# Kernel optimization log

Hardware: AMD Instinct MI355X
Metric: run time of the kernel (lower is better)

## Reference

```python
import jax, jax.numpy as jnp
import numpy as np

B, L, D, H, W = 2, 1024, 1024, 16, 64  # batch, length, dim, num_head, band_width
DH = D // H  # head_dim = 64


def setup_inputs() -> dict:
    key = jax.random.key(0)
    ks = jax.random.split(key, 7)
    scale = 0.02
    return {
        "x": jax.random.normal(ks[0], (B, L, D), dtype=jnp.float32),
        "Wq": jax.random.normal(ks[1], (D, D), dtype=jnp.float32) * scale,
        "Wk": jax.random.normal(ks[2], (D, D), dtype=jnp.float32) * scale,
        "Wv": jax.random.normal(ks[3], (D, D), dtype=jnp.float32) * scale,
        "Wo": jax.random.normal(ks[4], (D, D), dtype=jnp.float32) * scale,
        "last_k_init": jax.random.normal(ks[5], (W - 1, H, DH), dtype=jnp.float32),
        "last_v_init": jax.random.normal(ks[6], (W - 1, H, DH), dtype=jnp.float32),
    }


def reference(x, Wq, Wk, Wv, Wo, last_k_init, last_v_init):
    b, l, d = x.shape
    w1, h, dh = last_k_init.shape  # band_width-1, num_head, head_dim
    w = w1 + 1

    # torch nn.Linear: y = x @ W.T (no bias)
    q = (x @ Wq.T).reshape(b, l, h, dh)
    k = (x @ Wk.T).reshape(b, l, h, dh)
    v = (x @ Wv.T).reshape(b, l, h, dh)

    # prepend learned initial cache (fresh state: last_k is None)
    last_k = jnp.broadcast_to(last_k_init[None], (b, w1, h, dh))
    last_v = jnp.broadcast_to(last_v_init[None], (b, w1, h, dh))
    k_pad = jnp.concatenate([last_k, k], axis=1)  # [b, l+w-1, h, dh]
    v_pad = jnp.concatenate([last_v, v], axis=1)

    # query at position t attends offsets i in [0, w): key index t + i in padded
    # array == original position t - (w-1) + i  (causal sliding window of width w)
    idx = jnp.arange(l)[:, None] + jnp.arange(w)[None, :]  # [l, w]
    k_win = k_pad[:, idx]  # [b, l, w, h, dh]
    v_win = v_pad[:, idx]  # [b, l, w, h, dh]

    scores = jnp.einsum('blhd,blwhd->blwh', q, k_win) * (dh ** -0.5)
    attn = jax.nn.softmax(scores, axis=2)  # softmax over band offsets
    out = jnp.einsum('blwh,blwhd->blhd', attn, v_win).reshape(b, l, d)
    return out @ Wo.T
```

## Files before the change

### kernel.cpp

```cpp
#include <hip/hip_runtime.h>
#include <hip/hip_bf16.h>
#include <stdint.h>

#define B_ 2
#define L_ 1024
#define D_ 1024
#define H_ 16
#define W_ 64
#define DH_ 64

typedef __attribute__((ext_vector_type(8))) __bf16 bf16x8;
typedef __attribute__((ext_vector_type(4))) float floatx4;

#define AS3(p) ((__attribute__((address_space(3))) void*)(p))
#define AS1(p) ((const __attribute__((address_space(1))) void*)(p))

static __device__ __forceinline__ ushort f2bf(float f) {
    union { float f; uint32_t u; } v{f};
    uint32_t r = v.u + 0x7fff + ((v.u >> 16) & 1);
    return (ushort)(r >> 16);
}
static __device__ __forceinline__ uint32_t pack2(float a, float b) {
    return (uint32_t)f2bf(a) | ((uint32_t)f2bf(b) << 16);
}

__global__ __launch_bounds__(256) void cvt_inputs(
    const float* __restrict__ x, const float* __restrict__ wq, const float* __restrict__ wk,
    const float* __restrict__ wv, const float* __restrict__ wo,
    ushort* __restrict__ xb, ushort* __restrict__ wqb, ushort* __restrict__ wkb,
    ushort* __restrict__ wvb, ushort* __restrict__ wob) {
    const size_t M1 = 1u << 20;
    size_t i4 = ((size_t)blockIdx.x * 256 + threadIdx.x) * 4;
    const float* s; ushort* d; size_t off;
    if (i4 < 2 * M1)      { s = x;  d = xb;  off = i4; }
    else if (i4 < 3 * M1) { s = wq; d = wqb; off = i4 - 2 * M1; }
    else if (i4 < 4 * M1) { s = wk; d = wkb; off = i4 - 3 * M1; }
    else if (i4 < 5 * M1) { s = wv; d = wvb; off = i4 - 4 * M1; }
    else                  { s = wo; d = wob; off = i4 - 5 * M1; }
    float4 f = *(const float4*)(s + off);
    ushort4 o;
    o.x = f2bf(f.x); o.y = f2bf(f.y); o.z = f2bf(f.z); o.w = f2bf(f.w);
    *(ushort4*)(d + off) = o;
}

#define BK 64

__global__ __launch_bounds__(256) void gemm_qkv(
    const ushort* __restrict__ xb,
    const ushort* __restrict__ wqb, const ushort* __restrict__ wkb, const ushort* __restrict__ wvb,
    ushort* __restrict__ q, ushort* __restrict__ k, ushort* __restrict__ v) {
    __shared__ __align__(16) ushort As[128 * BK];
    __shared__ __align__(16) ushort Bs[64 * BK];
    const int tid = threadIdx.x;
    const int m0 = blockIdx.x * 128;
    const int nt = blockIdx.y;
    const int which = nt >> 4;
    const int n0 = (nt & 15) * 64;
    const ushort* wsel = which == 0 ? wqb : (which == 1 ? wkb : wvb);
    ushort* dsel = which == 0 ? q : (which == 1 ? k : v);

    const int lane = tid & 63;
    const int wv_ = tid >> 6;
    const int wm = (wv_ & 1) * 64;
    const int wn = (wv_ >> 1) * 32;
    const int lr = lane & 15;
    const int quad = lane >> 4;

    floatx4 acc[4][2];
#pragma unroll
    for (int i = 0; i < 4; ++i)
#pragma unroll
        for (int j = 0; j < 2; ++j) acc[i][j] = (floatx4){0.f, 0.f, 0.f, 0.f};

    int offA[4], offB[2];
#pragma unroll
    for (int it = 0; it < 4; ++it) {
        int c = tid + it * 256;
        int r = c >> 3, s = c & 7, g = s ^ (r & 7);
        offA[it] = (m0 + r) * 1024 + g * 8;
    }
#pragma unroll
    for (int it = 0; it < 2; ++it) {
        int c = tid + it * 256;
        int r = c >> 3, s = c & 7, g = s ^ (r & 7);
        offB[it] = (n0 + r) * 1024 + g * 8;
    }

    for (int k0 = 0; k0 < 1024; k0 += BK) {
#pragma unroll
        for (int it = 0; it < 4; ++it)
            __builtin_amdgcn_global_load_lds(AS1(xb + offA[it] + k0), AS3(As + (it * 256 + tid) * 8), 16, 0, 0);
#pragma unroll
        for (int it = 0; it < 2; ++it)
            __builtin_amdgcn_global_load_lds(AS1(wsel + offB[it] + k0), AS3(Bs + (it * 256 + tid) * 8), 16, 0, 0);
        __syncthreads();
#pragma unroll
        for (int ks = 0; ks < 2; ++ks) {
            bf16x8 af[4], bfr[2];
#pragma unroll
            for (int i = 0; i < 4; ++i) {
                int r = wm + i * 16 + lr;
                af[i] = *(const bf16x8*)(As + r * BK + (((ks * 4 + quad) ^ (r & 7)) * 8));
            }
#pragma unroll
            for (int j = 0; j < 2; ++j) {
                int r = wn + j * 16 + lr;
                bfr[j] = *(const bf16x8*)(Bs + r * BK + (((ks * 4 + quad) ^ (r & 7)) * 8));
            }
#pragma unroll
            for (int i = 0; i < 4; ++i)
#pragma unroll
                for (int j = 0; j < 2; ++j)
                    acc[i][j] = __builtin_amdgcn_mfma_f32_16x16x32_bf16(af[i], bfr[j], acc[i][j], 0, 0, 0);
        }
        __syncthreads();
    }

#pragma unroll
    for (int i = 0; i < 4; ++i) {
        int rbase = m0 + wm + i * 16 + quad * 4;
#pragma unroll
        for (int j = 0; j < 2; ++j) {
            int c = n0 + wn + j * 16 + lr;
            int h = c >> 6, dh = c & 63;
#pragma unroll
            for (int r = 0; r < 4; ++r) {
                int m = rbase + r;
                int bb = m >> 10, l = m & 1023;
                dsel[(((size_t)bb * 16 + h) * 1024 + l) * 64 + dh] = f2bf(acc[i][j][r]);
            }
        }
    }
}

__global__ __launch_bounds__(256) void gemm_wo(
    const ushort* __restrict__ ab,
    const ushort* __restrict__ wob,
    float* __restrict__ out) {
    __shared__ __align__(16) ushort As[64 * BK];
    __shared__ __align__(16) ushort Bs[64 * BK];
    const int tid = threadIdx.x;
    const int m0 = blockIdx.x * 64;
    const int n0 = blockIdx.y * 64;
    const int lane = tid & 63;
    const int wv_ = tid >> 6;
    const int wm = wv_ * 16;
    const int lr = lane & 15;
    const int quad = lane >> 4;

    floatx4 acc[4];
#pragma unroll
    for (int j = 0; j < 4; ++j) acc[j] = (floatx4){0.f, 0.f, 0.f, 0.f};

    int offA[2], offB[2];
#pragma unroll
    for (int it = 0; it < 2; ++it) {
        int c = tid + it * 256;
        int r = c >> 3, s = c & 7, g = s ^ (r & 7);
        offA[it] = (m0 + r) * 1024 + g * 8;
        offB[it] = (n0 + r) * 1024 + g * 8;
    }

    for (int k0 = 0; k0 < 1024; k0 += BK) {
#pragma unroll
        for (int it = 0; it < 2; ++it)
            __builtin_amdgcn_global_load_lds(AS1(ab + offA[it] + k0), AS3(As + (it * 256 + tid) * 8), 16, 0, 0);
#pragma unroll
        for (int it = 0; it < 2; ++it)
            __builtin_amdgcn_global_load_lds(AS1(wob + offB[it] + k0), AS3(Bs + (it * 256 + tid) * 8), 16, 0, 0);
        __syncthreads();
#pragma unroll
        for (int ks = 0; ks < 2; ++ks) {
            int ra = wm + lr;
            bf16x8 af = *(const bf16x8*)(As + ra * BK + (((ks * 4 + quad) ^ (ra & 7)) * 8));
            bf16x8 bfr[4];
#pragma unroll
            for (int j = 0; j < 4; ++j) {
                int r = j * 16 + lr;
                bfr[j] = *(const bf16x8*)(Bs + r * BK + (((ks * 4 + quad) ^ (r & 7)) * 8));
            }
#pragma unroll
            for (int j = 0; j < 4; ++j)
                acc[j] = __builtin_amdgcn_mfma_f32_16x16x32_bf16(af, bfr[j], acc[j], 0, 0, 0);
        }
        __syncthreads();
    }

#pragma unroll
    for (int j = 0; j < 4; ++j) {
        int c = n0 + j * 16 + lr;
#pragma unroll
        for (int r = 0; r < 4; ++r) {
            int m = m0 + wm + quad * 4 + r;
            out[(size_t)m * 1024 + c] = acc[j][r];
        }
    }
}

#define STRQ 72
#define STRV 136

__global__ __launch_bounds__(256) void band_attn3(
    const ushort* __restrict__ q,
    const ushort* __restrict__ k,
    const ushort* __restrict__ v,
    const float* __restrict__ lastk,
    const float* __restrict__ lastv,
    ushort* __restrict__ ao) {
    __shared__ __align__(16) ushort Qs[64 * STRQ];
    __shared__ __align__(16) ushort Kw[128 * STRQ];
    __shared__ __align__(16) ushort Vt[64 * STRV];
    __shared__ __align__(16) ushort Ps[64 * STRV];
    const int tid = threadIdx.x;
    const int lane = tid & 63;
    const int wid = tid >> 6;
    const int l0 = blockIdx.x * 64;
    const int b = blockIdx.y >> 4, h = blockIdx.y & 15;
    const size_t hb = (size_t)(b * 16 + h) * 1024 * 64;

#pragma unroll
    for (int it = 0; it < 2; ++it) {
        int c = tid + it * 256;
        int rr = c >> 3, cc = (c & 7) * 8;
        *(uint4*)(Qs + rr * STRQ + cc) = *(const uint4*)(q + hb + (size_t)(l0 + rr) * 64 + cc);
    }
#pragma unroll
    for (int it = 0; it < 4; ++it) {
        int c = tid + it * 256;
        int j = c >> 3, cc = (c & 7) * 8;
        int pos = l0 + j - 63;
        uint4 t = {0u, 0u, 0u, 0u};
        if (j < 127) {
            if (pos >= 0) {
                t = *(const uint4*)(k + hb + (size_t)pos * 64 + cc);
            } else {
                const float* sk = lastk + ((size_t)j * 16 + h) * 64 + cc;
                float4 a0 = *(const float4*)sk, a1 = *(const float4*)(sk + 4);
                t.x = pack2(a0.x, a0.y); t.y = pack2(a0.z, a0.w);
                t.z = pack2(a1.x, a1.y); t.w = pack2(a1.z, a1.w);
            }
        }
        *(uint4*)(Kw + j * STRQ + cc) = t;
    }
#pragma unroll
    for (int it = 0; it < 4; ++it) {
        int c = tid + it * 256;
        int j = c >> 3, d8 = (c & 7) * 8;
        int pos = l0 + j - 63;
        ushort tv[8];
        if (j >= 127) {
#pragma unroll
            for (int t = 0; t < 8; ++t) tv[t] = 0;
        } else if (pos >= 0) {
            union { uint4 u4; ushort us[8]; } tu;
            tu.u4 = *(const uint4*)(v + hb + (size_t)pos * 64 + d8);
#pragma unroll
            for (int t = 0; t < 8; ++t) tv[t] = tu.us[t];
        } else {
            const float* sv = lastv + ((size_t)j * 16 + h) * 64 + d8;
#pragma unroll
            for (int t = 0; t < 8; ++t) tv[t] = f2bf(sv[t]);
        }
#pragma unroll
        for (int t = 0; t < 8; ++t) Vt[(size_t)(d8 + t) * STRV + j] = tv[t];
    }
    __syncthreads();

    const int lr = lane & 15;
    const int quad = lane >> 4;

    floatx4 sa[8];
#pragma unroll
    for (int nt = 0; nt < 8; ++nt) sa[nt] = (floatx4){0.f, 0.f, 0.f, 0.f};
    bf16x8 aq[2];
#pragma unroll
    for (int ks = 0; ks < 2; ++ks)
        aq[ks] = *(const bf16x8*)(Qs + (wid * 16 + lr) * STRQ + ks * 32 + quad * 8);
#pragma unroll
    for (int ks = 0; ks < 2; ++ks)
#pragma unroll
        for (int nt = 0; nt < 8; ++nt) {
            bf16x8 bk = *(const bf16x8*)(Kw + (nt * 16 + lr) * STRQ + ks * 32 + quad * 8);
            sa[nt] = __builtin_amdgcn_mfma_f32_16x16x32_bf16(aq[ks], bk, sa[nt], 0, 0, 0);
        }

#pragma unroll
    for (int rr = 0; rr < 4; ++rr) {
        int i_loc = wid * 16 + quad * 4 + rr;
        float sv[8];
        float mv = -1e30f;
#pragma unroll
        for (int nt = 0; nt < 8; ++nt) {
            int j = nt * 16 + lr;
            int w = j - i_loc;
            sv[nt] = (w >= 0 && w < 64) ? sa[nt][rr] * 0.125f : -1e30f;
            mv = fmaxf(mv, sv[nt]);
        }
#pragma unroll
        for (int off = 8; off; off >>= 1) mv = fmaxf(mv, __shfl_xor(mv, off, 16));
        float sum = 0.f;
#pragma unroll
        for (int nt = 0; nt < 8; ++nt) {
            sv[nt] = __expf(sv[nt] - mv);
            sum += sv[nt];
        }
#pragma unroll
        for (int off = 8; off; off >>= 1) sum += __shfl_xor(sum, off, 16);
        float inv = 1.f / sum;
#pragma unroll
        for (int nt = 0; nt < 8; ++nt)
            Ps[(size_t)i_loc * STRV + nt * 16 + lr] = f2bf(sv[nt] * inv);
    }

    floatx4 oa[4];
#pragma unroll
    for (int nt = 0; nt < 4; ++nt) oa[nt] = (floatx4){0.f, 0.f, 0.f, 0.f};
#pragma unroll
    for (int ks = 0; ks < 4; ++ks) {
        bf16x8 ap = *(const bf16x8*)(Ps + (wid * 16 + lr) * STRV + ks * 32 + quad * 8);
#pragma unroll
        for (int nt = 0; nt < 4; ++nt) {
            bf16x8 bv = *(const bf16x8*)(Vt + (nt * 16 + lr) * STRV + ks * 32 + quad * 8);
            oa[nt] = __builtin_amdgcn_mfma_f32_16x16x32_bf16(ap, bv, oa[nt], 0, 0, 0);
        }
    }

#pragma unroll
    for (int nt = 0; nt < 4; ++nt) {
        int d = nt * 16 + lr;
#pragma unroll
        for (int rr = 0; rr < 4; ++rr) {
            int i_loc = wid * 16 + quad * 4 + rr;
            ao[((size_t)b * 1024 + l0 + i_loc) * 1024 + h * 64 + d] = f2bf(oa[nt][rr]);
        }
    }
}

extern "C" void kernel_launch(void* const* d_in, const int* in_sizes, int n_in,
                              void* d_out, int out_size, void* d_ws, size_t ws_size,
                              hipStream_t stream) {
    const float* x     = (const float*)d_in[0];
    const float* Wq    = (const float*)d_in[1];
    const float* Wk    = (const float*)d_in[2];
    const float* Wv    = (const float*)d_in[3];
    const float* Wo    = (const float*)d_in[4];
    const float* lastk = (const float*)d_in[5];
    const float* lastv = (const float*)d_in[6];
    float* out = (float*)d_out;

    const size_t M1 = 1u << 20;
    ushort* xb  = (ushort*)d_ws;
    ushort* wqb = xb + 2 * M1;
    ushort* wkb = wqb + M1;
    ushort* wvb = wkb + M1;
    ushort* wob = wvb + M1;
    ushort* qh  = wob + M1;
    ushort* kh  = qh + 2 * M1;
    ushort* vh  = kh + 2 * M1;
    ushort* ao  = vh + 2 * M1;

    cvt_inputs<<<6144, 256, 0, stream>>>(x, Wq, Wk, Wv, Wo, xb, wqb, wkb, wvb, wob);
    gemm_qkv<<<dim3(16, 48), 256, 0, stream>>>(xb, wqb, wkb, wvb, qh, kh, vh);
    band_attn3<<<dim3(16, 32), 256, 0, stream>>>(qh, kh, vh, lastk, lastv, ao);
    gemm_wo<<<dim3(32, 16), 256, 0, stream>>>(ao, wob, out);
}
```

Baseline: 121.2 us.

## Fuse all four stages into one cooperative persistent kernel with grid syncs

Result: slower. 400.4 us (+230.4%).

```diff
diff --git a/kernel.cpp b/kernel.cpp
--- a/kernel.cpp
+++ b/kernel.cpp
@@ -1,6 +1,9 @@
 #include <hip/hip_runtime.h>
 #include <hip/hip_bf16.h>
+#include <hip/hip_cooperative_groups.h>
 #include <stdint.h>
+
+namespace cg = cooperative_groups;
 
 #define B_ 2
 #define L_ 1024
@@ -8,6 +11,8 @@
 #define H_ 16
 #define W_ 64
 #define DH_ 64
+#define NB 768
+#define BK 64
 
 typedef __attribute__((ext_vector_type(8))) __bf16 bf16x8;
 typedef __attribute__((ext_vector_type(4))) float floatx4;
@@ -22,6 +27,319 @@
 }
 static __device__ __forceinline__ uint32_t pack2(float a, float b) {
     return (uint32_t)f2bf(a) | ((uint32_t)f2bf(b) << 16);
+}
+
+#define STRQ 72
+#define STRV 136
+
+struct GemmSm { ushort A[128 * BK]; ushort B[64 * BK]; };
+struct WoSm   { ushort A[64 * BK];  ushort B[64 * BK]; };
+struct AttnScores { ushort Qs[64 * STRQ]; ushort Kw[128 * STRQ]; };
+union  AttnOv { AttnScores s; ushort Ps[64 * STRV]; };
+struct AttnSm { ushort Vt[64 * STRV]; AttnOv ov; };
+union  Smem { GemmSm g; WoSm w; AttnSm a; };
+
+__global__ __launch_bounds__(256, 3) void fused_all(
+    const float* __restrict__ x,  const float* __restrict__ Wq, const float* __restrict__ Wk,
+    const float* __restrict__ Wv, const float* __restrict__ Wo,
+    const float* __restrict__ lastk, const float* __restrict__ lastv,
+    float* __restrict__ out, ushort* __restrict__ ws) {
+    __shared__ __align__(16) Smem sm;
+    cg::grid_group grid = cg::this_grid();
+
+    const int tid = threadIdx.x;
+    const int bid = blockIdx.x;
+    const int lane = tid & 63;
+    const int wid = tid >> 6;
+    const int lr = lane & 15;
+    const int quad = lane >> 4;
+
+    const size_t M1 = 1u << 20;
+    ushort* xb  = ws;
+    ushort* wqb = xb + 2 * M1;
+    ushort* wkb = wqb + M1;
+    ushort* wvb = wkb + M1;
+    ushort* wob = wvb + M1;
+    ushort* qh  = wob + M1;
+    ushort* kh  = qh + 2 * M1;
+    ushort* vh  = kh + 2 * M1;
+    ushort* ao  = vh + 2 * M1;
+
+    {
+        const size_t total4 = 6 * M1 / 4;
+        for (size_t c = (size_t)bid * 256 + tid; c < total4; c += (size_t)NB * 256) {
+            size_t i4 = c * 4;
+            const float* s; ushort* d; size_t off;
+            if (i4 < 2 * M1)      { s = x;  d = xb;  off = i4; }
+            else if (i4 < 3 * M1) { s = Wq; d = wqb; off = i4 - 2 * M1; }
+            else if (i4 < 4 * M1) { s = Wk; d = wkb; off = i4 - 3 * M1; }
+            else if (i4 < 5 * M1) { s = Wv; d = wvb; off = i4 - 4 * M1; }
+            else                  { s = Wo; d = wob; off = i4 - 5 * M1; }
+            float4 f = *(const float4*)(s + off);
+            ushort4 o;
+            o.x = f2bf(f.x); o.y = f2bf(f.y); o.z = f2bf(f.z); o.w = f2bf(f.w);
+            *(ushort4*)(d + off) = o;
+        }
+    }
+    grid.sync();
+
+    {
+        const int m0 = (bid & 15) * 128;
+        const int nt = bid >> 4;
+        const int which = nt >> 4;
+        const int n0 = (nt & 15) * 64;
+        const ushort* wsel = which == 0 ? wqb : (which == 1 ? wkb : wvb);
+        ushort* dsel = which == 0 ? qh : (which == 1 ? kh : vh);
+        const int wm = (wid & 1) * 64;
+        const int wn = (wid >> 1) * 32;
+
+        floatx4 acc[4][2];
+#pragma unroll
+        for (int i = 0; i < 4; ++i)
+#pragma unroll
+            for (int j = 0; j < 2; ++j) acc[i][j] = (floatx4){0.f, 0.f, 0.f, 0.f};
+
+        int offA[4], offB[2];
+#pragma unroll
+        for (int it = 0; it < 4; ++it) {
+            int c = tid + it * 256;
+            int r = c >> 3, s = c & 7, g = s ^ (r & 7);
+            offA[it] = (m0 + r) * 1024 + g * 8;
+        }
+#pragma unroll
+        for (int it = 0; it < 2; ++it) {
+            int c = tid + it * 256;
+            int r = c >> 3, s = c & 7, g = s ^ (r & 7);
+            offB[it] = (n0 + r) * 1024 + g * 8;
+        }
+
+        for (int k0 = 0; k0 < 1024; k0 += BK) {
+#pragma unroll
+            for (int it = 0; it < 4; ++it)
+                __builtin_amdgcn_global_load_lds(AS1(xb + offA[it] + k0), AS3(sm.g.A + (it * 256 + tid) * 8), 16, 0, 0);
+#pragma unroll
+            for (int it = 0; it < 2; ++it)
+                __builtin_amdgcn_global_load_lds(AS1(wsel + offB[it] + k0), AS3(sm.g.B + (it * 256 + tid) * 8), 16, 0, 0);
+            __syncthreads();
+#pragma unroll
+            for (int ks = 0; ks < 2; ++ks) {
+                bf16x8 af[4], bfr[2];
+#pragma unroll
+                for (int i = 0; i < 4; ++i) {
+                    int r = wm + i * 16 + lr;
+                    af[i] = *(const bf16x8*)(sm.g.A + r * BK + (((ks * 4 + quad) ^ (r & 7)) * 8));
+                }
+#pragma unroll
+                for (int j = 0; j < 2; ++j) {
+                    int r = wn + j * 16 + lr;
+                    bfr[j] = *(const bf16x8*)(sm.g.B + r * BK + (((ks * 4 + quad) ^ (r & 7)) * 8));
+                }
+#pragma unroll
+                for (int i = 0; i < 4; ++i)
+#pragma unroll
+                    for (int j = 0; j < 2; ++j)
+                        acc[i][j] = __builtin_amdgcn_mfma_f32_16x16x32_bf16(af[i], bfr[j], acc[i][j], 0, 0, 0);
+            }
+            __syncthreads();
+        }
+
+#pragma unroll
+        for (int i = 0; i < 4; ++i) {
+            int rbase = m0 + wm + i * 16 + quad * 4;
+#pragma unroll
+            for (int j = 0; j < 2; ++j) {
+                int c = n0 + wn + j * 16 + lr;
+                int h = c >> 6, dh = c & 63;
+#pragma unroll
+                for (int r = 0; r < 4; ++r) {
+                    int m = rbase + r;
+                    int bb = m >> 10, l = m & 1023;
+                    dsel[(((size_t)bb * 16 + h) * 1024 + l) * 64 + dh] = f2bf(acc[i][j][r]);
+                }
+            }
+        }
+    }
+    grid.sync();
+
+    if (bid < 512) {
+        const int l0 = (bid & 15) * 64;
+        const int b = bid >> 8, h = (bid >> 4) & 15;
+        const size_t hb = (size_t)(b * 16 + h) * 1024 * 64;
+        ushort* Qs = sm.a.ov.s.Qs;
+        ushort* Kw = sm.a.ov.s.Kw;
+        ushort* Vt = sm.a.Vt;
+        ushort* Ps = sm.a.ov.Ps;
+
+#pragma unroll
+        for (int it = 0; it < 2; ++it) {
+            int c = tid + it * 256;
+            int rr = c >> 3, cc = (c & 7) * 8;
+            *(uint4*)(Qs + rr * STRQ + cc) = *(const uint4*)(qh + hb + (size_t)(l0 + rr) * 64 + cc);
+        }
+#pragma unroll
+        for (int it = 0; it < 4; ++it) {
+            int c = tid + it * 256;
+            int j = c >> 3, cc = (c & 7) * 8;
+            int pos = l0 + j - 63;
+            uint4 t = {0u, 0u, 0u, 0u};
+            if (j < 127) {
+                if (pos >= 0) {
+                    t = *(const uint4*)(kh + hb + (size_t)pos * 64 + cc);
+                } else {
+                    const float* sk = lastk + ((size_t)j * 16 + h) * 64 + cc;
+                    float4 a0 = *(const float4*)sk, a1 = *(const float4*)(sk + 4);
+                    t.x = pack2(a0.x, a0.y); t.y = pack2(a0.z, a0.w);
+                    t.z = pack2(a1.x, a1.y); t.w = pack2(a1.z, a1.w);
+                }
+            }
+            *(uint4*)(Kw + j * STRQ + cc) = t;
+        }
+#pragma unroll
+        for (int it = 0; it < 4; ++it) {
+            int c = tid + it * 256;
+            int j = c >> 3, d8 = (c & 7) * 8;
+            int pos = l0 + j - 63;
+            ushort tv[8];
+            if (j >= 127) {
+#pragma unroll
+                for (int t = 0; t < 8; ++t) tv[t] = 0;
+            } else if (pos >= 0) {
+                union { uint4 u4; ushort us[8]; } tu;
+                tu.u4 = *(const uint4*)(vh + hb + (size_t)pos * 64 + d8);
+#pragma unroll
+                for (int t = 0; t < 8; ++t) tv[t] = tu.us[t];
+            } else {
+                const float* sv = lastv + ((size_t)j * 16 + h) * 64 + d8;
+#pragma unroll
+                for (int t = 0; t < 8; ++t) tv[t] = f2bf(sv[t]);
+            }
+#pragma unroll
+            for (int t = 0; t < 8; ++t) Vt[(size_t)(d8 + t) * STRV + j] = tv[t];
+        }
+        __syncthreads();
+
+        floatx4 sa[8];
+#pragma unroll
+        for (int nt = 0; nt < 8; ++nt) sa[nt] = (floatx4){0.f, 0.f, 0.f, 0.f};
+        bf16x8 aq[2];
+#pragma unroll
+        for (int ks = 0; ks < 2; ++ks)
+            aq[ks] = *(const bf16x8*)(Qs + (wid * 16 + lr) * STRQ + ks * 32 + quad * 8);
+#pragma unroll
+        for (int ks = 0; ks < 2; ++ks)
+#pragma unroll
+            for (int nt = 0; nt < 8; ++nt) {
+                bf16x8 bk = *(const bf16x8*)(Kw + (nt * 16 + lr) * STRQ + ks * 32 + quad * 8);
+                sa[nt] = __builtin_amdgcn_mfma_f32_16x16x32_bf16(aq[ks], bk, sa[nt], 0, 0, 0);
+            }
+        __syncthreads();
+
+#pragma unroll
+        for (int rr = 0; rr < 4; ++rr) {
+            int i_loc = wid * 16 + quad * 4 + rr;
+            float svv[8];
+            float mv = -1e30f;
+#pragma unroll
+            for (int nt = 0; nt < 8; ++nt) {
+                int j = nt * 16 + lr;
+                int w = j - i_loc;
+                svv[nt] = (w >= 0 && w < 64) ? sa[nt][rr] * 0.125f : -1e30f;
+                mv = fmaxf(mv, svv[nt]);
+            }
+#pragma unroll
+            for (int off = 8; off; off >>= 1) mv = fmaxf(mv, __shfl_xor(mv, off, 16));
+            float sum = 0.f;
+#pragma unroll
+            for (int nt = 0; nt < 8; ++nt) {
+                svv[nt] = __expf(svv[nt] - mv);
+                sum += svv[nt];
+            }
+#pragma unroll
+            for (int off = 8; off; off >>= 1) sum += __shfl_xor(sum, off, 16);
+            float inv = 1.f / sum;
+#pragma unroll
+            for (int nt = 0; nt < 8; ++nt)
+                Ps[(size_t)i_loc * STRV + nt * 16 + lr] = f2bf(svv[nt] * inv);
+        }
+
+        floatx4 oa[4];
+#pragma unroll
+        for (int nt = 0; nt < 4; ++nt) oa[nt] = (floatx4){0.f, 0.f, 0.f, 0.f};
+#pragma unroll
+        for (int ks = 0; ks < 4; ++ks) {
+            bf16x8 ap = *(const bf16x8*)(Ps + (wid * 16 + lr) * STRV + ks * 32 + quad * 8);
+#pragma unroll
+            for (int nt = 0; nt < 4; ++nt) {
+                bf16x8 bv = *(const bf16x8*)(Vt + (nt * 16 + lr) * STRV + ks * 32 + quad * 8);
+                oa[nt] = __builtin_amdgcn_mfma_f32_16x16x32_bf16(ap, bv, oa[nt], 0, 0, 0);
+            }
+        }
+
+#pragma unroll
+        for (int nt = 0; nt < 4; ++nt) {
+            int d = nt * 16 + lr;
+#pragma unroll
+            for (int rr = 0; rr < 4; ++rr) {
+                int i_loc = wid * 16 + quad * 4 + rr;
+                ao[((size_t)b * 1024 + l0 + i_loc) * 1024 + h * 64 + d] = f2bf(oa[nt][rr]);
+            }
+        }
+    }
+    grid.sync();
+
+    if (bid < 512) {
+        const int m0 = (bid >> 4) * 64;
+        const int n0 = (bid & 15) * 64;
+        const int wm = wid * 16;
+
+        floatx4 acc[4];
+#pragma unroll
+        for (int j = 0; j < 4; ++j) acc[j] = (floatx4){0.f, 0.f, 0.f, 0.f};
+
+        int offA[2], offB[2];
+#pragma unroll
+        for (int it = 0; it < 2; ++it) {
+            int c = tid + it * 256;
+            int r = c >> 3, s = c & 7, g = s ^ (r & 7);
+            offA[it] = (m0 + r) * 1024 + g * 8;
+            offB[it] = (n0 + r) * 1024 + g * 8;
+        }
+
+        for (int k0 = 0; k0 < 1024; k0 += BK) {
+#pragma unroll
+            for (int it = 0; it < 2; ++it)
+                __builtin_amdgcn_global_load_lds(AS1(ao + offA[it] + k0), AS3(sm.w.A + (it * 256 + tid) * 8), 16, 0, 0);
+#pragma unroll
+            for (int it = 0; it < 2; ++it)
+                __builtin_amdgcn_global_load_lds(AS1(wob + offB[it] + k0), AS3(sm.w.B + (it * 256 + tid) * 8), 16, 0, 0);
+            __syncthreads();
+#pragma unroll
+            for (int ks = 0; ks < 2; ++ks) {
+                int ra = wm + lr;
+                bf16x8 af = *(const bf16x8*)(sm.w.A + ra * BK + (((ks * 4 + quad) ^ (ra & 7)) * 8));
+                bf16x8 bfr[4];
+#pragma unroll
+                for (int j = 0; j < 4; ++j) {
+                    int r = j * 16 + lr;
+                    bfr[j] = *(const bf16x8*)(sm.w.B + r * BK + (((ks * 4 + quad) ^ (r & 7)) * 8));
+                }
+#pragma unroll
+                for (int j = 0; j < 4; ++j)
+                    acc[j] = __builtin_amdgcn_mfma_f32_16x16x32_bf16(af, bfr[j], acc[j], 0, 0, 0);
+            }
+            __syncthreads();
+        }
+
+#pragma unroll
+        for (int j = 0; j < 4; ++j) {
+            int c = n0 + j * 16 + lr;
+#pragma unroll
+            for (int r = 0; r < 4; ++r) {
+                int m = m0 + wm + quad * 4 + r;
+                out[(size_t)m * 1024 + c] = acc[j][r];
+            }
+        }
+    }
 }
 
 __global__ __launch_bounds__(256) void cvt_inputs(
@@ -43,8 +361,6 @@
     *(ushort4*)(d + off) = o;
 }
 
-#define BK 64
-
 __global__ __launch_bounds__(256) void gemm_qkv(
     const ushort* __restrict__ xb,
     const ushort* __restrict__ wqb, const ushort* __restrict__ wkb, const ushort* __restrict__ wvb,
@@ -58,7 +374,6 @@
     const int n0 = (nt & 15) * 64;
     const ushort* wsel = which == 0 ? wqb : (which == 1 ? wkb : wvb);
     ushort* dsel = which == 0 ? q : (which == 1 ? k : v);
-
     const int lane = tid & 63;
     const int wv_ = tid >> 6;
     const int wm = (wv_ & 1) * 64;
@@ -134,9 +449,7 @@
 }
 
 __global__ __launch_bounds__(256) void gemm_wo(
-    const ushort* __restrict__ ab,
-    const ushort* __restrict__ wob,
-    float* __restrict__ out) {
+    const ushort* __restrict__ ab, const ushort* __restrict__ wob, float* __restrict__ out) {
     __shared__ __align__(16) ushort As[64 * BK];
     __shared__ __align__(16) ushort Bs[64 * BK];
     const int tid = threadIdx.x;
@@ -197,15 +510,9 @@
     }
 }
 
-#define STRQ 72
-#define STRV 136
-
 __global__ __launch_bounds__(256) void band_attn3(
-    const ushort* __restrict__ q,
-    const ushort* __restrict__ k,
-    const ushort* __restrict__ v,
-    const float* __restrict__ lastk,
-    const float* __restrict__ lastv,
+    const ushort* __restrict__ q, const ushort* __restrict__ k, const ushort* __restrict__ v,
+    const float* __restrict__ lastk, const float* __restrict__ lastv,
     ushort* __restrict__ ao) {
     __shared__ __align__(16) ushort Qs[64 * STRQ];
     __shared__ __align__(16) ushort Kw[128 * STRQ];
@@ -287,29 +594,29 @@
 #pragma unroll
     for (int rr = 0; rr < 4; ++rr) {
         int i_loc = wid * 16 + quad * 4 + rr;
-        float sv[8];
+        float svv[8];
         float mv = -1e30f;
 #pragma unroll
         for (int nt = 0; nt < 8; ++nt) {
             int j = nt * 16 + lr;
             int w = j - i_loc;
-            sv[nt] = (w >= 0 && w < 64) ? sa[nt][rr] * 0.125f : -1e30f;
-            mv = fmaxf(mv, sv[nt]);
+            svv[nt] = (w >= 0 && w < 64) ? sa[nt][rr] * 0.125f : -1e30f;
+            mv = fmaxf(mv, svv[nt]);
         }
 #pragma unroll
         for (int off = 8; off; off >>= 1) mv = fmaxf(mv, __shfl_xor(mv, off, 16));
         float sum = 0.f;
 #pragma unroll
         for (int nt = 0; nt < 8; ++nt) {
-            sv[nt] = __expf(sv[nt] - mv);
-            sum += sv[nt];
+            svv[nt] = __expf(svv[nt] - mv);
+            sum += svv[nt];
         }
 #pragma unroll
         for (int off = 8; off; off >>= 1) sum += __shfl_xor(sum, off, 16);
         float inv = 1.f / sum;
 #pragma unroll
         for (int nt = 0; nt < 8; ++nt)
-            Ps[(size_t)i_loc * STRV + nt * 16 + lr] = f2bf(sv[nt] * inv);
+            Ps[(size_t)i_loc * STRV + nt * 16 + lr] = f2bf(svv[nt] * inv);
     }
 
     floatx4 oa[4];
@@ -347,20 +654,26 @@
     const float* lastk = (const float*)d_in[5];
     const float* lastv = (const float*)d_in[6];
     float* out = (float*)d_out;
-
-    const size_t M1 = 1u << 20;
-    ushort* xb  = (ushort*)d_ws;
-    ushort* wqb = xb + 2 * M1;
-    ushort* wkb = wqb + M1;
-    ushort* wvb = wkb + M1;
-    ushort* wob = wvb + M1;
-    ushort* qh  = wob + M1;
-    ushort* kh  = qh + 2 * M1;
-    ushort* vh  = kh + 2 * M1;
-    ushort* ao  = vh + 2 * M1;
-
-    cvt_inputs<<<6144, 256, 0, stream>>>(x, Wq, Wk, Wv, Wo, xb, wqb, wkb, wvb, wob);
-    gemm_qkv<<<dim3(16, 48), 256, 0, stream>>>(xb, wqb, wkb, wvb, qh, kh, vh);
-    band_attn3<<<dim3(16, 32), 256, 0, stream>>>(qh, kh, vh, lastk, lastv, ao);
-    gemm_wo<<<dim3(32, 16), 256, 0, stream>>>(ao, wob, out);
-}
+    ushort* ws = (ushort*)d_ws;
+
+    void* args[] = {(void*)&x, (void*)&Wq, (void*)&Wk, (void*)&Wv, (void*)&Wo,
+                    (void*)&lastk, (void*)&lastv, (void*)&out, (void*)&ws};
+    hipError_t err = hipLaunchCooperativeKernel((const void*)fused_all, dim3(NB), dim3(256),
+                                                args, 0, stream);
+    if (err != hipSuccess) {
+        const size_t M1 = 1u << 20;
+        ushort* xb  = ws;
+        ushort* wqb = xb + 2 * M1;
+        ushort* wkb = wqb + M1;
+        ushort* wvb = wkb + M1;
+        ushort* wob = wvb + M1;
+        ushort* qh  = wob + M1;
+        ushort* kh  = qh + 2 * M1;
+        ushort* vh  = kh + 2 * M1;
+        ushort* ao  = vh + 2 * M1;
+        cvt_inputs<<<6144, 256, 0, stream>>>(x, Wq, Wk, Wv, Wo, xb, wqb, wkb, wvb, wob);
+        gemm_qkv<<<dim3(16, 48), 256, 0, stream>>>(xb, wqb, wkb, wvb, qh, kh, vh);
+        band_attn3<<<dim3(16, 32), 256, 0, stream>>>(qh, kh, vh, lastk, lastv, ao);
+        gemm_wo<<<dim3(32, 16), 256, 0, stream>>>(ao, wob, out);
+    }
+}
```
